# Performance work log

Hardware: AMD Instinct MI355X
Metric: run time of the kernel (lower is better)

## Reference

```python
import jax, jax.numpy as jnp
import numpy as np

N_BLADES = 8      # 2**len(sig_g), sig_g=[1,1,1]
N_EP_STEPS = 3
STEP_SIZE = 0.01
B, IN_DIM, OUT_DIM = 1024, 4096, 2048
HID = OUT_DIM * N_BLADES


def setup_inputs() -> dict:
    key = jax.random.key(0)
    k0, k1, k2, k3, k4, k5 = jax.random.split(key, 6)
    x = jax.random.normal(k0, (B, IN_DIM), jnp.float32)
    # input_proj: Linear(in_dim, out_dim*n_blades)
    W_in = jax.random.normal(k1, (IN_DIM, HID), jnp.float32) / np.sqrt(IN_DIM)
    b_in = jax.random.normal(k2, (HID,), jnp.float32) * 0.01
    # energy interaction matrix W: (n_blades, n_blades), init * 0.1
    W_e = jax.random.normal(k3, (N_BLADES, N_BLADES), jnp.float32) * 0.1
    # output_proj: Linear(out_dim*n_blades, out_dim)
    W_out = jax.random.normal(k4, (HID, OUT_DIM), jnp.float32) / np.sqrt(HID)
    b_out = jax.random.normal(k5, (OUT_DIM,), jnp.float32) * 0.01
    return {"x": x, "W_in": W_in, "b_in": b_in, "W_e": W_e,
            "W_out": W_out, "b_out": b_out}


def reference(x, W_in, b_in, W_e, W_out, b_out):
    # h: (B, out_dim, n_blades)
    h = (x @ W_in + b_in).reshape(x.shape[0], OUT_DIM, N_BLADES)
    # EP relaxation: analytic dE/dh = h + 0.1 * h @ (W + W^T)
    # (torch computed this via autograd on a detached copy each step,
    #  so the gradient term carries no graph -> stop_gradient)
    W_sym = W_e + W_e.T
    for _ in range(N_EP_STEPS):
        grad = jax.lax.stop_gradient(h + 0.1 * (h @ W_sym))
        h = h - STEP_SIZE * grad
    h_flat = h.reshape(x.shape[0], HID)
    return h_flat @ W_out + b_out
```

## Files before the change

kernel.cpp:

```cpp
#include <hip/hip_runtime.h>
#include <stdint.h>

#define AS1 __attribute__((address_space(1)))
#define AS3 __attribute__((address_space(3)))

typedef float v4f __attribute__((ext_vector_type(4)));
typedef __bf16 v8bf __attribute__((ext_vector_type(8)));
typedef __bf16 bf16x4 __attribute__((ext_vector_type(4)));

static_assert(sizeof(v8bf) == 16, "v8bf must be 16B");
static_assert(sizeof(bf16x4) == 8, "bf16x4 must be 8B");

__device__ __forceinline__ unsigned short f2bf(float f) {
  unsigned int x = __float_as_uint(f);
  x += 0x7fffu + ((x >> 16) & 1u);
  return (unsigned short)(x >> 16);
}

__device__ __forceinline__ void async16(void* lds, const void* g) {
  __builtin_amdgcn_global_load_lds((const AS1 unsigned int*)g,
                                   (AS3 unsigned int*)lds, 16, 0, 0);
}


__global__ void prep_m3_kernel(const float* __restrict__ We, float* __restrict__ m3) {
  __shared__ float Ms[64], M2[64];
  int t = threadIdx.x;
  int i = t >> 3, j = t & 7;
  float wsym = We[i * 8 + j] + We[j * 8 + i];
  Ms[t] = (i == j ? 0.99f : 0.0f) - 0.001f * wsym;
  __syncthreads();
  float s = 0.f;
#pragma unroll
  for (int p = 0; p < 8; ++p) s += Ms[i * 8 + p] * Ms[p * 8 + j];
  M2[t] = s;
  __syncthreads();
  s = 0.f;
#pragma unroll
  for (int p = 0; p < 8; ++p) s += M2[i * 8 + p] * Ms[p * 8 + j];
  m3[t] = s;
}

__global__ void cvt_bf16_kernel(const float* __restrict__ in, unsigned short* __restrict__ out) {
  int i = (blockIdx.x * 256 + threadIdx.x) * 8;
  float4 a = *(const float4*)(in + i);
  float4 b = *(const float4*)(in + i + 4);
  alignas(16) unsigned short r[8] = {f2bf(a.x), f2bf(a.y), f2bf(a.z), f2bf(a.w),
                                     f2bf(b.x), f2bf(b.y), f2bf(b.z), f2bf(b.w)};
  *(uint4*)(out + i) = *(const uint4*)r;
}

__global__ void fold_h_kernel(unsigned short* __restrict__ h, const float* __restrict__ m3) {
  __shared__ float m3s[64];
  int t = threadIdx.x;
  if (t < 64) m3s[t] = m3[t];
  __syncthreads();
  size_t g = ((size_t)blockIdx.x * 256 + t) * 8;
  uint4 raw = *(const uint4*)(h + g);
  const unsigned short* rp = (const unsigned short*)&raw;
  float v[8];
#pragma unroll
  for (int p = 0; p < 8; ++p) v[p] = __uint_as_float((unsigned int)rp[p] << 16);
  alignas(16) unsigned short o[8];
#pragma unroll
  for (int j = 0; j < 8; ++j) {
    float s = 0.f;
#pragma unroll
    for (int p = 0; p < 8; ++p) s += v[p] * m3s[p * 8 + j];
    o[j] = f2bf(s);
  }
  *(uint4*)(h + g) = *(const uint4*)o;
}

template <bool OUT_BF16, bool SPLITK>
__global__ __launch_bounds__(512, 1) void gemm256f_kernel(
    const unsigned short* __restrict__ A, const float* __restrict__ Bsrc,
    const float* __restrict__ bias, void* __restrict__ Cout,
    int M, int N, int K, int ldkA, int ldnB) {
  __shared__ char ldsc[131072];

  const int flat = blockIdx.x + gridDim.x * (blockIdx.y + gridDim.y * blockIdx.z);
  const int xcd = flat & 7, idx = flat >> 3;
  int bn, bm, bz;
  if (SPLITK) { bz = xcd; bn = idx & 7; bm = idx >> 3; }
  else        { bz = 0;   bn = xcd * 8 + (idx & 7); bm = idx >> 3; }
  const int m0 = bm * 256, n0 = bn * 256;
  const int kb = SPLITK ? bz * K : 0;

  const int t = threadIdx.x;
  const int lane = t & 63, w = t >> 6;
  const int wr = w >> 2, wn = w & 3;
  const int r16 = lane & 15, kc = lane >> 4;
  const int xorv = (r16 & 7) << 4;
  const int acol0 = (kc << 4) ^ xorv;
  const int acol1 = ((4 | kc) << 4) ^ xorv;
  const int abase = wr * 16384 + r16 * 128;
  const int bbase = 32768 + wn * 8192 + r16 * 128;

  const int srow = w * 8 + (lane >> 3);
  const int scol = ((lane & 7) ^ (lane >> 3)) * 8;
  const int sdst = w * 1024 + lane * 16;
  const unsigned short* gAp = A + (size_t)(m0 + srow) * ldkA + kb + scol;

  const int n0s = 4 * lane;
  const int rotc = (lane >> 1) & 3;
  const float* gB = Bsrc + (size_t)(kb + w * 4) * ldnB + n0 + n0s;

  v4f acc[8][4];
#pragma unroll
  for (int mi = 0; mi < 8; ++mi)
#pragma unroll
    for (int nj = 0; nj < 4; ++nj) acc[mi][nj] = (v4f){0.f, 0.f, 0.f, 0.f};

  float4 L[2][4];

#define STAGE_A(OB)                                                        \
  _Pragma("unroll") for (int i = 0; i < 4; ++i)                            \
      async16(ldsc + (OB) + i * 8192 + sdst, gAp + (size_t)(i * 64) * ldkA);
#define LOAD_BGLB()                                                        \
  _Pragma("unroll") for (int ii = 0; ii < 2; ++ii)                         \
      _Pragma("unroll") for (int j = 0; j < 4; ++j)                        \
          L[ii][j] = *(const float4*)(gB + (size_t)(ii * 32 + j) * ldnB);
#define CVT_WRITE_B(OB)                                                          \
  _Pragma("unroll") for (int ii = 0; ii < 2; ++ii) {                             \
    const int k4 = w * 4 + ii * 32;                                              \
    bf16x4 R0 = (bf16x4){(__bf16)L[ii][0].x, (__bf16)L[ii][1].x,                 \
                         (__bf16)L[ii][2].x, (__bf16)L[ii][3].x};                \
    bf16x4 R1 = (bf16x4){(__bf16)L[ii][0].y, (__bf16)L[ii][1].y,                 \
                         (__bf16)L[ii][2].y, (__bf16)L[ii][3].y};                \
    bf16x4 R2 = (bf16x4){(__bf16)L[ii][0].z, (__bf16)L[ii][1].z,                 \
                         (__bf16)L[ii][2].z, (__bf16)L[ii][3].z};                \
    bf16x4 R3 = (bf16x4){(__bf16)L[ii][0].w, (__bf16)L[ii][1].w,                 \
                         (__bf16)L[ii][2].w, (__bf16)L[ii][3].w};                \
    _Pragma("unroll") for (int d = 0; d < 4; ++d) {                              \
      int o = (d + rotc) & 3;                                                    \
      int row = n0s + o;                                                         \
      bf16x4 vv = (o & 2) ? ((o & 1) ? R3 : R2) : ((o & 1) ? R1 : R0);           \
      *(bf16x4*)(ldsc + (OB) + 32768 + row * 128 +                               \
                 ((((k4 >> 3) ^ (row & 7)) << 4) | ((k4 & 7) << 1))) = vv;       \
    }                                                                            \
  }
#define LOAD_A(BB, MH)                                                     \
  _Pragma("unroll") for (int m = 0; m < 4; ++m) {                          \
    a[m * 2 + 0] = *(const v8bf*)(ldsc + (BB) + abase + (MH) * 8192 + m * 2048 + acol0); \
    a[m * 2 + 1] = *(const v8bf*)(ldsc + (BB) + abase + (MH) * 8192 + m * 2048 + acol1); \
  }
#define LOAD_B(BB, NH, BR)                                                 \
  _Pragma("unroll") for (int n = 0; n < 2; ++n) {                          \
    BR[n * 2 + 0] = *(const v8bf*)(ldsc + (BB) + bbase + (NH) * 4096 + n * 2048 + acol0); \
    BR[n * 2 + 1] = *(const v8bf*)(ldsc + (BB) + bbase + (NH) * 4096 + n * 2048 + acol1); \
  }
#define MFMA_QUAD(MH, NH, BR)                                              \
  _Pragma("unroll") for (int m = 0; m < 4; ++m) {                          \
    _Pragma("unroll") for (int n = 0; n < 2; ++n) {                        \
      acc[(MH) * 4 + m][(NH) * 2 + n] = __builtin_amdgcn_mfma_f32_16x16x32_bf16( \
          a[m * 2 + 0], BR[n * 2 + 0], acc[(MH) * 4 + m][(NH) * 2 + n], 0, 0, 0); \
      acc[(MH) * 4 + m][(NH) * 2 + n] = __builtin_amdgcn_mfma_f32_16x16x32_bf16( \
          a[m * 2 + 1], BR[n * 2 + 1], acc[(MH) * 4 + m][(NH) * 2 + n], 0, 0, 0); \
    }                                                                      \
  }

  const int NT = K >> 6;

  STAGE_A(0);
  LOAD_BGLB();
  gAp += 64;
  CVT_WRITE_B(0);
  if (NT > 1) gB += (size_t)64 * ldnB;
  LOAD_BGLB();
  if (NT > 2) gB += (size_t)64 * ldnB;
  asm volatile("s_waitcnt vmcnt(8) lgkmcnt(0)" ::: "memory");
  __builtin_amdgcn_s_barrier();

  int buf = 0;
  for (int tt = 0; tt < NT; ++tt) {
    const int bb = buf << 16;
    const int ob = (buf ^ 1) << 16;
    const bool pf = (tt + 1 < NT);

    if (pf) {
      CVT_WRITE_B(ob);
      STAGE_A(ob);
      gAp += 64;
    }
    LOAD_BGLB();
    if (tt + 3 < NT) gB += (size_t)64 * ldnB;
    __builtin_amdgcn_sched_barrier(0);

    {
      v8bf a[8], b0r[4], b1r[4];
      LOAD_A(bb, 0);
      LOAD_B(bb, 0, b0r);
      LOAD_B(bb, 1, b1r);
      __builtin_amdgcn_s_setprio(1);
      MFMA_QUAD(0, 0, b0r);
      MFMA_QUAD(0, 1, b1r);
      __builtin_amdgcn_s_setprio(0);
      LOAD_A(bb, 1);
      __builtin_amdgcn_s_setprio(1);
      MFMA_QUAD(1, 1, b1r);
      MFMA_QUAD(1, 0, b0r);
      __builtin_amdgcn_s_setprio(0);
    }
    __builtin_amdgcn_sched_barrier(0);

    asm volatile("s_waitcnt vmcnt(8) lgkmcnt(0)" ::: "memory");
    __builtin_amdgcn_s_barrier();
    buf ^= 1;
  }

  float* Cp = (float*)Cout + (SPLITK ? (size_t)bz * M * N : 0);
#pragma unroll
  for (int mi = 0; mi < 8; ++mi) {
    int grow = m0 + wr * 128 + mi * 16 + kc * 4;
#pragma unroll
    for (int nj = 0; nj < 4; ++nj) {
      int gcol = n0 + wn * 64 + nj * 16 + r16;
      float bv = SPLITK ? 0.f : bias[gcol];
#pragma unroll
      for (int j = 0; j < 4; ++j) {
        float v = acc[mi][nj][j] + bv;
        size_t idxo = (size_t)(grow + j) * N + gcol;
        if (OUT_BF16)
          ((unsigned short*)Cout)[idxo] = f2bf(v);
        else
          Cp[idxo] = v;
      }
    }
  }
#undef STAGE_A
#undef LOAD_BGLB
#undef CVT_WRITE_B
#undef LOAD_A
#undef LOAD_B
#undef MFMA_QUAD
}

__global__ void reduce_splitk_kernel(const float* __restrict__ part,
                                     const float* __restrict__ bias,
                                     float* __restrict__ out, int MN, int N, int S) {
  int i = (blockIdx.x * 256 + threadIdx.x) * 4;
  float4 s = *(const float4*)(part + i);
  for (int k = 1; k < S; ++k) {
    float4 v = *(const float4*)(part + (size_t)k * MN + i);
    s.x += v.x; s.y += v.y; s.z += v.z; s.w += v.w;
  }
  int n = i & (N - 1);
  const float4 bv = *(const float4*)(bias + n);
  s.x += bv.x; s.y += bv.y; s.z += bv.z; s.w += bv.w;
  *(float4*)(out + i) = s;
}


extern "C" void kernel_launch(void* const* d_in, const int* in_sizes, int n_in,
                              void* d_out, int out_size, void* d_ws, size_t ws_size,
                              hipStream_t stream) {
  const float* x     = (const float*)d_in[0];
  const float* W_in  = (const float*)d_in[1];
  const float* b_in  = (const float*)d_in[2];
  const float* W_e   = (const float*)d_in[3];
  const float* W_out = (const float*)d_in[4];
  const float* b_out = (const float*)d_in[5];
  float* out = (float*)d_out;

  char* ws = (char*)d_ws;
  const size_t OFF_M3 = 0;
  const size_t OFF_X  = 1ull << 20;
  const size_t OFF_H  = 10ull << 20;
  const size_t OFF_P  = 48ull << 20;
  float* m3          = (float*)(ws + OFF_M3);
  unsigned short* xb = (unsigned short*)(ws + OFF_X);
  unsigned short* h  = (unsigned short*)(ws + OFF_H);
  float* part        = (float*)(ws + OFF_P);

  prep_m3_kernel<<<1, 64, 0, stream>>>(W_e, m3);
  cvt_bf16_kernel<<<2048, 256, 0, stream>>>(x, xb);

  gemm256f_kernel<true, false><<<dim3(64, 4), 512, 0, stream>>>(
      xb, W_in, b_in, h, 1024, 16384, 4096, 4096, 16384);

  fold_h_kernel<<<8192, 256, 0, stream>>>(h, m3);

  gemm256f_kernel<false, true><<<dim3(8, 4, 8), 512, 0, stream>>>(
      h, W_out, nullptr, part, 1024, 2048, 2048, 16384, 2048);

  reduce_splitk_kernel<<<2048, 256, 0, stream>>>(part, b_out, out, 1024 * 2048, 2048, 8);
}
```

Before: 263.9 us.

## Load A operand directly from global into registers, dropping LDS staging

The A operand tiles are now read straight from global memory into MFMA register fragments instead of being staged asynchronously into LDS and read back. LDS use is halved to hold only the converted B tiles, and the vmcnt waits are removed from the barrier sync. This removes the LDS round-trip and barrier dependency for A. In exchange, each wave loads A redundantly across the four wn waves, the global loads are strided and poorly coalesced, and the load latency sits right before the MFMAs with no prefetch.

```diff
diff --git a/kernel.cpp b/kernel.cpp
--- a/kernel.cpp
+++ b/kernel.cpp
@@ -1,8 +1,5 @@
 #include <hip/hip_runtime.h>
 #include <stdint.h>
-
-#define AS1 __attribute__((address_space(1)))
-#define AS3 __attribute__((address_space(3)))
 
 typedef float v4f __attribute__((ext_vector_type(4)));
 typedef __bf16 v8bf __attribute__((ext_vector_type(8)));
@@ -15,11 +12,6 @@
   unsigned int x = __float_as_uint(f);
   x += 0x7fffu + ((x >> 16) & 1u);
   return (unsigned short)(x >> 16);
-}
-
-__device__ __forceinline__ void async16(void* lds, const void* g) {
-  __builtin_amdgcn_global_load_lds((const AS1 unsigned int*)g,
-                                   (AS3 unsigned int*)lds, 16, 0, 0);
 }
 
 
@@ -77,7 +69,7 @@
     const unsigned short* __restrict__ A, const float* __restrict__ Bsrc,
     const float* __restrict__ bias, void* __restrict__ Cout,
     int M, int N, int K, int ldkA, int ldnB) {
-  __shared__ char ldsc[131072];
+  __shared__ char ldsc[65536];
 
   const int flat = blockIdx.x + gridDim.x * (blockIdx.y + gridDim.y * blockIdx.z);
   const int xcd = flat & 7, idx = flat >> 3;
@@ -94,13 +86,10 @@
   const int xorv = (r16 & 7) << 4;
   const int acol0 = (kc << 4) ^ xorv;
   const int acol1 = ((4 | kc) << 4) ^ xorv;
-  const int abase = wr * 16384 + r16 * 128;
-  const int bbase = 32768 + wn * 8192 + r16 * 128;
-
-  const int srow = w * 8 + (lane >> 3);
-  const int scol = ((lane & 7) ^ (lane >> 3)) * 8;
-  const int sdst = w * 1024 + lane * 16;
-  const unsigned short* gAp = A + (size_t)(m0 + srow) * ldkA + kb + scol;
+  const int bbase = wn * 8192 + r16 * 128;
+
+  const unsigned short* gA =
+      A + (size_t)(m0 + wr * 128 + r16) * ldkA + kb + kc * 8;
 
   const int n0s = 4 * lane;
   const int rotc = (lane >> 1) & 3;
@@ -114,9 +103,12 @@
 
   float4 L[2][4];
 
-#define STAGE_A(OB)                                                        \
-  _Pragma("unroll") for (int i = 0; i < 4; ++i)                            \
-      async16(ldsc + (OB) + i * 8192 + sdst, gAp + (size_t)(i * 64) * ldkA);
+#define LOAD_AG(MH)                                                        \
+  _Pragma("unroll") for (int m = 0; m < 4; ++m) {                          \
+    const unsigned short* p = gA + (size_t)((MH) * 64 + m * 16) * ldkA;    \
+    a[m * 2 + 0] = *(const v8bf*)p;                                        \
+    a[m * 2 + 1] = *(const v8bf*)(p + 32);                                 \
+  }
 #define LOAD_BGLB()                                                        \
   _Pragma("unroll") for (int ii = 0; ii < 2; ++ii)                         \
       _Pragma("unroll") for (int j = 0; j < 4; ++j)                        \
@@ -136,14 +128,9 @@
       int o = (d + rotc) & 3;                                                    \
       int row = n0s + o;                                                         \
       bf16x4 vv = (o & 2) ? ((o & 1) ? R3 : R2) : ((o & 1) ? R1 : R0);           \
-      *(bf16x4*)(ldsc + (OB) + 32768 + row * 128 +                               \
+      *(bf16x4*)(ldsc + (OB) + row * 128 +                                       \
                  ((((k4 >> 3) ^ (row & 7)) << 4) | ((k4 & 7) << 1))) = vv;       \
     }                                                                            \
-  }
-#define LOAD_A(BB, MH)                                                     \
-  _Pragma("unroll") for (int m = 0; m < 4; ++m) {                          \
-    a[m * 2 + 0] = *(const v8bf*)(ldsc + (BB) + abase + (MH) * 8192 + m * 2048 + acol0); \
-    a[m * 2 + 1] = *(const v8bf*)(ldsc + (BB) + abase + (MH) * 8192 + m * 2048 + acol1); \
   }
 #define LOAD_B(BB, NH, BR)                                                 \
   _Pragma("unroll") for (int n = 0; n < 2; ++n) {                          \
@@ -162,50 +149,43 @@
 
   const int NT = K >> 6;
 
-  STAGE_A(0);
   LOAD_BGLB();
-  gAp += 64;
   CVT_WRITE_B(0);
   if (NT > 1) gB += (size_t)64 * ldnB;
   LOAD_BGLB();
   if (NT > 2) gB += (size_t)64 * ldnB;
-  asm volatile("s_waitcnt vmcnt(8) lgkmcnt(0)" ::: "memory");
+  asm volatile("s_waitcnt lgkmcnt(0)" ::: "memory");
   __builtin_amdgcn_s_barrier();
 
   int buf = 0;
   for (int tt = 0; tt < NT; ++tt) {
-    const int bb = buf << 16;
-    const int ob = (buf ^ 1) << 16;
+    const int bb = buf << 15;
+    const int ob = (buf ^ 1) << 15;
     const bool pf = (tt + 1 < NT);
-
-    if (pf) {
-      CVT_WRITE_B(ob);
-      STAGE_A(ob);
-      gAp += 64;
-    }
+    v8bf a[8], b0r[4], b1r[4];
+
+    LOAD_AG(0);
+    if (pf) { CVT_WRITE_B(ob); }
     LOAD_BGLB();
     if (tt + 3 < NT) gB += (size_t)64 * ldnB;
     __builtin_amdgcn_sched_barrier(0);
 
-    {
-      v8bf a[8], b0r[4], b1r[4];
-      LOAD_A(bb, 0);
-      LOAD_B(bb, 0, b0r);
-      LOAD_B(bb, 1, b1r);
-      __builtin_amdgcn_s_setprio(1);
-      MFMA_QUAD(0, 0, b0r);
-      MFMA_QUAD(0, 1, b1r);
-      __builtin_amdgcn_s_setprio(0);
-      LOAD_A(bb, 1);
-      __builtin_amdgcn_s_setprio(1);
-      MFMA_QUAD(1, 1, b1r);
-      MFMA_QUAD(1, 0, b0r);
-      __builtin_amdgcn_s_setprio(0);
-    }
+    LOAD_B(bb, 0, b0r);
+    LOAD_B(bb, 1, b1r);
+    __builtin_amdgcn_s_setprio(1);
+    MFMA_QUAD(0, 0, b0r);
+    MFMA_QUAD(0, 1, b1r);
+    __builtin_amdgcn_s_setprio(0);
+    LOAD_AG(1);
+    __builtin_amdgcn_s_setprio(1);
+    MFMA_QUAD(1, 1, b1r);
+    MFMA_QUAD(1, 0, b0r);
+    __builtin_amdgcn_s_setprio(0);
     __builtin_amdgcn_sched_barrier(0);
 
-    asm volatile("s_waitcnt vmcnt(8) lgkmcnt(0)" ::: "memory");
+    asm volatile("s_waitcnt lgkmcnt(0)" ::: "memory");
     __builtin_amdgcn_s_barrier();
+    gA += 64;
     buf ^= 1;
   }
 
@@ -228,10 +208,9 @@
       }
     }
   }
-#undef STAGE_A
+#undef LOAD_AG
 #undef LOAD_BGLB
 #undef CVT_WRITE_B
-#undef LOAD_A
 #undef LOAD_B
 #undef MFMA_QUAD
 }
```

After: 522.7 us. 1.98x slower.
